# Optimization experiments

Hardware: AMD Instinct MI355X
Metric: run time of the kernel (lower is better)

## Reference

```python
import jax, jax.numpy as jnp
import numpy as np

N_STEPS = 1000
LR_INNER = 0.1
LOG_CLAMP = -100.0  # torch BCE clamps log terms at -100


def _mlp(params, x):
    h = jax.nn.sigmoid(x @ params['w1'].T + params['b1'])   # [4,16]
    return jax.nn.sigmoid(h @ params['w2'].T + params['b2'])  # [4,1]


def _bce(y_pred, y_true):
    lp = jnp.clip(jnp.log(y_pred), LOG_CLAMP)
    lq = jnp.clip(jnp.log(1.0 - y_pred), LOG_CLAMP)
    return -jnp.mean(y_true * lp + (1.0 - y_true) * lq)


def setup_inputs() -> dict:
    key = jax.random.key(0)
    k1, k2 = jax.random.split(key)
    x = jnp.array([[0.0, 0.0], [0.0, 1.0], [1.0, 0.0], [1.0, 1.0]], dtype=jnp.float32)
    y_true = jnp.array([[0.0], [1.0], [1.0], [0.0]], dtype=jnp.float32)
    return {
        'x': x,
        'y_true': y_true,
        'w1': jax.random.normal(k1, (16, 2), dtype=jnp.float32),
        'b1': jnp.zeros((16,), dtype=jnp.float32),
        'w2': jax.random.normal(k2, (1, 16), dtype=jnp.float32),
        'b2': jnp.zeros((1,), dtype=jnp.float32),
    }


def reference(x, y_true, w1, b1, w2, b2):
    params = {'w1': w1, 'b1': b1, 'w2': w2, 'b2': b2}

    def loss_fn(p):
        return _bce(_mlp(p, x), y_true)

    def step(p, _):
        loss, grads = jax.value_and_grad(loss_fn)(p)
        p_new = jax.tree_util.tree_map(lambda a, g: a - LR_INNER * g, p, grads)  # sgd
        return p_new, loss

    params, losses = jax.lax.scan(step, params, None, length=N_STEPS)
    final_output = _mlp(params, x)  # [4,1]
    return final_output, losses
```

## Files before the change

### kernel.cpp

```cpp
#include <hip/hip_runtime.h>
#include <hip/hip_bf16.h>

#define N_STEPS 1000

#define DOT_STAGE(x, N) do { float _o;                                         \
    asm("s_nop 1\n\t"                                                          \
        "v_add_f32_dpp %0, %1, %1 row_ror:" #N " row_mask:0xf bank_mask:0xf"   \
        : "=v"(_o) : "v"(x));                                                  \
    x = _o; } while (0)

#define QSUM5(q0, q1, q2, q3, q4) \
    asm("s_nop 1\n\t"                                                             \
        "v_add_f32_dpp %0, %0, %0 quad_perm:[1,0,3,2] row_mask:0xf bank_mask:0xf\n\t" \
        "v_add_f32_dpp %1, %1, %1 quad_perm:[1,0,3,2] row_mask:0xf bank_mask:0xf\n\t" \
        "v_add_f32_dpp %2, %2, %2 quad_perm:[1,0,3,2] row_mask:0xf bank_mask:0xf\n\t" \
        "v_add_f32_dpp %3, %3, %3 quad_perm:[1,0,3,2] row_mask:0xf bank_mask:0xf\n\t" \
        "v_add_f32_dpp %4, %4, %4 quad_perm:[1,0,3,2] row_mask:0xf bank_mask:0xf\n\t" \
        "v_add_f32_dpp %0, %0, %0 quad_perm:[2,3,0,1] row_mask:0xf bank_mask:0xf\n\t" \
        "v_add_f32_dpp %1, %1, %1 quad_perm:[2,3,0,1] row_mask:0xf bank_mask:0xf\n\t" \
        "v_add_f32_dpp %2, %2, %2 quad_perm:[2,3,0,1] row_mask:0xf bank_mask:0xf\n\t" \
        "v_add_f32_dpp %3, %3, %3 quad_perm:[2,3,0,1] row_mask:0xf bank_mask:0xf\n\t" \
        "v_add_f32_dpp %4, %4, %4 quad_perm:[2,3,0,1] row_mask:0xf bank_mask:0xf"     \
        : "+v"(q0), "+v"(q1), "+v"(q2), "+v"(q3), "+v"(q4))

#if defined(__has_builtin)
#  if __has_builtin(__builtin_amdgcn_permlane32_swap) && __has_builtin(__builtin_amdgcn_permlane16_swap)
#    define HAVE_PL 1
#  endif
#endif
#ifndef HAVE_PL
#  define HAVE_PL 0
#endif

template<bool PL> static __device__ __forceinline__ float redswap16(float x) {
    if (PL) {
#if HAVE_PL
        auto r = __builtin_amdgcn_permlane16_swap(__float_as_uint(x), __float_as_uint(x), false, false);
        return __uint_as_float(r[0]) + __uint_as_float(r[1]);
#endif
    }
    return x + __shfl_xor(x, 16);
}
template<bool PL> static __device__ __forceinline__ float redswap32(float x) {
    if (PL) {
#if HAVE_PL
        auto r = __builtin_amdgcn_permlane32_swap(__float_as_uint(x), __float_as_uint(x), false, false);
        return __uint_as_float(r[0]) + __uint_as_float(r[1]);
#endif
    }
    return x + __shfl_xor(x, 32);
}

#define NEG_LOG2E (-1.4426950408889634f)
#define LRS       (0.14426950408889634f)

template<bool PL>
static __device__ __forceinline__ void run_all(
    int tid, float Xr0, float Xr1, float cr,
    float Y0, float Y1, float Y2, float Y3,
    float z1s, float w2s, float B,
    float* __restrict__ p_lds, float* __restrict__ out)
{
    const float lrs_seed = (tid < 4) ? LRS : 0.0f;
    const float nC  = -0.1f;
    const float nX0 = -0.1f * Xr0;
    const float nX1 = -0.1f * Xr1;

    #pragma unroll 2
    for (int s = 0; s < N_STEPS; ++s) {
        float e1 = __builtin_amdgcn_exp2f(z1s);
        float h  = __builtin_amdgcn_rcpf(1.0f + e1);
        float vp  = (w2s * h) * (1.0f - h);
        float vX0 = vp * Xr0;
        float vX1 = vp * Xr1;

        float t = fmaf(h, w2s, B);
        DOT_STAGE(t, 4);
        DOT_STAGE(t, 8);
        t = redswap16<PL>(t);
        t = redswap32<PL>(t);
        float e2 = __builtin_amdgcn_exp2f(t);
        float p  = __builtin_amdgcn_rcpf(1.0f + e2);

        p_lds[4 * s + (tid & 3)] = p;

        float d  = fmaf(0.25f, p, cr);
        float dh = d * h;
        float u  = d * vp;
        float a0 = d * vX0;
        float a1 = d * vX1;
        QSUM5(d, dh, u, a0, a1);

        w2s = fmaf(LRS,      dh, w2s);
        B   = fmaf(lrs_seed, d,  B);
        z1s = fmaf(nC,  u,  z1s);
        z1s = fmaf(nX0, a0, z1s);
        z1s = fmaf(nX1, a1, z1s);
    }

    {
        float e1 = __builtin_amdgcn_exp2f(z1s);
        float h  = __builtin_amdgcn_rcpf(1.0f + e1);
        float t  = fmaf(h, w2s, B);
        DOT_STAGE(t, 4);
        DOT_STAGE(t, 8);
        t = redswap16<PL>(t);
        t = redswap32<PL>(t);
        float p = __builtin_amdgcn_rcpf(1.0f + __builtin_amdgcn_exp2f(t));
        if (tid < 4) out[tid] = p;
    }

    __syncthreads();

    for (int s2 = tid; s2 < N_STEPS; s2 += 64) {
        const float4 pv = *(const float4*)&p_lds[s2 * 4];
        float pp[4] = {pv.x, pv.y, pv.z, pv.w};
        float yy[4] = {Y0, Y1, Y2, Y3};
        float sum = 0.0f;
        #pragma unroll
        for (int i = 0; i < 4; ++i) {
            float pi = pp[i];
            float qi = 1.0f - pi;
            float lp = fmaxf(__logf(pi), -100.0f);
            float lq = fmaxf(__logf(qi), -100.0f);
            sum += yy[i] * lp + (1.0f - yy[i]) * lq;
        }
        out[4 + s2] = -(sum * 0.25f);
    }
}

__global__ __launch_bounds__(64, 1) void xor_train_v8(
    const void* __restrict__ x_p,
    const void* __restrict__ y_p,
    const void* __restrict__ w1_p,
    const void* __restrict__ s16a_p,
    const void* __restrict__ s16b_p,
    const void* __restrict__ b2_p,
    float* __restrict__ out)
{
    __shared__ float p_lds[N_STEPS * 4];

    const int tid = threadIdx.x;
    const int r   = tid & 3;
    const int j   = tid >> 2;

    const bool in_bf16 = (((const float*)y_p)[1] != 1.0f);
    const bool a_is_b1 = (((const unsigned*)s16a_p)[0] == 0u);
    const void* b1_p = a_is_b1 ? s16a_p : s16b_p;
    const void* w2_p = a_is_b1 ? s16b_p : s16a_p;

    float X[4][2], Y[4];
    float w10, w11, b1v, w2v, b2v;
    if (in_bf16) {
        const __hip_bfloat16* xb = (const __hip_bfloat16*)x_p;
        const __hip_bfloat16* yb = (const __hip_bfloat16*)y_p;
        #pragma unroll
        for (int i = 0; i < 4; ++i) {
            X[i][0] = __bfloat162float(xb[2 * i + 0]);
            X[i][1] = __bfloat162float(xb[2 * i + 1]);
            Y[i]    = __bfloat162float(yb[i]);
        }
        const __hip_bfloat16* w1b = (const __hip_bfloat16*)w1_p;
        w10 = __bfloat162float(w1b[2 * j + 0]);
        w11 = __bfloat162float(w1b[2 * j + 1]);
        b1v = __bfloat162float(((const __hip_bfloat16*)b1_p)[j]);
        w2v = __bfloat162float(((const __hip_bfloat16*)w2_p)[j]);
        b2v = __bfloat162float(((const __hip_bfloat16*)b2_p)[0]);
    } else {
        const float* xf = (const float*)x_p;
        const float* yf = (const float*)y_p;
        #pragma unroll
        for (int i = 0; i < 4; ++i) {
            X[i][0] = xf[2 * i + 0];
            X[i][1] = xf[2 * i + 1];
            Y[i]    = yf[i];
        }
        w10 = ((const float*)w1_p)[2 * j + 0];
        w11 = ((const float*)w1_p)[2 * j + 1];
        b1v = ((const float*)b1_p)[j];
        w2v = ((const float*)w2_p)[j];
        b2v = ((const float*)b2_p)[0];
    }

    const float Xr0 = X[r][0], Xr1 = X[r][1];
    const float cr  = -0.25f * Y[r];

    const float z1u = fmaf(Xr1, w11, fmaf(Xr0, w10, b1v));
    const float z1s = NEG_LOG2E * z1u;
    const float w2s = NEG_LOG2E * w2v;
    const float B   = (tid < 4) ? (NEG_LOG2E * b2v) : 0.0f;

    bool pl_ok = false;
#if HAVE_PL
    {
        float tv = (float)(1 << (tid >> 4));
        float fs = redswap32<true>(redswap16<true>(tv));
        pl_ok = (bool)__all(fs == 15.0f);
    }
#endif

    if (pl_ok)
        run_all<true>(tid, Xr0, Xr1, cr, Y[0], Y[1], Y[2], Y[3],
                      z1s, w2s, B, p_lds, out);
    else
        run_all<false>(tid, Xr0, Xr1, cr, Y[0], Y[1], Y[2], Y[3],
                       z1s, w2s, B, p_lds, out);
}

extern "C" void kernel_launch(void* const* d_in, const int* in_sizes, int n_in,
                              void* d_out, int out_size, void* d_ws, size_t ws_size,
                              hipStream_t stream) {
    const void* xv = nullptr; const void* yv = nullptr; const void* w1 = nullptr;
    const void* b2 = nullptr;
    const void* s16[2] = {nullptr, nullptr}; int n16 = 0;
    for (int i = 0; i < n_in; ++i) {
        switch (in_sizes[i]) {
            case 8:  xv = d_in[i]; break;
            case 4:  yv = d_in[i]; break;
            case 32: w1 = d_in[i]; break;
            case 1:  b2 = d_in[i]; break;
            case 16: if (n16 < 2) s16[n16++] = d_in[i]; break;
            default: break;
        }
    }
    if (!xv || !yv || !w1 || !b2 || n16 != 2) {
        xv = d_in[0]; yv = d_in[1]; w1 = d_in[2];
        s16[0] = d_in[3]; s16[1] = d_in[4]; b2 = d_in[5];
    }
    float* out = (float*)d_out;

    hipLaunchKernelGGL(xor_train_v8, dim3(1), dim3(64), 0, stream,
                       xv, yv, w1, s16[0], s16[1], b2, out);
}
```

Before: 118.0 us.

## Update hidden pre-activations via input Gram matrix instead of reducing gradients

Replaces the quad-wide reductions of the w1/b1 gradient terms with rotated copies of the per-row backprop term, combined through precomputed coefficients 1+x_r·x_i. This tracks the pre-activation z1 directly in input space, cutting the number of cross-lane DPP adds per step from ten to four plus three movs. It trades cross-lane reductions for an extra FMA and extra registers, and may change the rounding order slightly.

```diff
diff --git a/kernel.cpp b/kernel.cpp
--- a/kernel.cpp
+++ b/kernel.cpp
@@ -9,19 +9,18 @@
         : "=v"(_o) : "v"(x));                                                  \
     x = _o; } while (0)
 
-#define QSUM5(q0, q1, q2, q3, q4) \
-    asm("s_nop 1\n\t"                                                             \
-        "v_add_f32_dpp %0, %0, %0 quad_perm:[1,0,3,2] row_mask:0xf bank_mask:0xf\n\t" \
-        "v_add_f32_dpp %1, %1, %1 quad_perm:[1,0,3,2] row_mask:0xf bank_mask:0xf\n\t" \
-        "v_add_f32_dpp %2, %2, %2 quad_perm:[1,0,3,2] row_mask:0xf bank_mask:0xf\n\t" \
-        "v_add_f32_dpp %3, %3, %3 quad_perm:[1,0,3,2] row_mask:0xf bank_mask:0xf\n\t" \
-        "v_add_f32_dpp %4, %4, %4 quad_perm:[1,0,3,2] row_mask:0xf bank_mask:0xf\n\t" \
-        "v_add_f32_dpp %0, %0, %0 quad_perm:[2,3,0,1] row_mask:0xf bank_mask:0xf\n\t" \
-        "v_add_f32_dpp %1, %1, %1 quad_perm:[2,3,0,1] row_mask:0xf bank_mask:0xf\n\t" \
-        "v_add_f32_dpp %2, %2, %2 quad_perm:[2,3,0,1] row_mask:0xf bank_mask:0xf\n\t" \
-        "v_add_f32_dpp %3, %3, %3 quad_perm:[2,3,0,1] row_mask:0xf bank_mask:0xf\n\t" \
-        "v_add_f32_dpp %4, %4, %4 quad_perm:[2,3,0,1] row_mask:0xf bank_mask:0xf"     \
-        : "+v"(q0), "+v"(q1), "+v"(q2), "+v"(q3), "+v"(q4))
+#define BWD_XLANE(d, dh, u, u1, u2, u3) \
+    asm("s_nop 1\n\t"                                                                  \
+        "v_add_f32_dpp %[d_], %[d_], %[d_] quad_perm:[1,0,3,2] row_mask:0xf bank_mask:0xf\n\t" \
+        "v_mov_b32_dpp %[u1_], %[u_] quad_perm:[1,2,3,0] row_mask:0xf bank_mask:0xf\n\t"       \
+        "v_add_f32_dpp %[h_], %[h_], %[h_] quad_perm:[1,0,3,2] row_mask:0xf bank_mask:0xf\n\t" \
+        "v_mov_b32_dpp %[u2_], %[u_] quad_perm:[2,3,0,1] row_mask:0xf bank_mask:0xf\n\t"       \
+        "v_mov_b32_dpp %[u3_], %[u_] quad_perm:[3,0,1,2] row_mask:0xf bank_mask:0xf\n\t"       \
+        "v_add_f32_dpp %[d_], %[d_], %[d_] quad_perm:[2,3,0,1] row_mask:0xf bank_mask:0xf\n\t" \
+        "v_add_f32_dpp %[h_], %[h_], %[h_] quad_perm:[2,3,0,1] row_mask:0xf bank_mask:0xf"     \
+        : [d_] "+v"(d), [h_] "+v"(dh),                                                 \
+          [u1_] "=&v"(u1), [u2_] "=&v"(u2), [u3_] "=&v"(u3)                            \
+        : [u_] "v"(u))
 
 #if defined(__has_builtin)
 #  if __has_builtin(__builtin_amdgcn_permlane32_swap) && __has_builtin(__builtin_amdgcn_permlane16_swap)
@@ -57,22 +56,18 @@
 template<bool PL>
 static __device__ __forceinline__ void run_all(
     int tid, float Xr0, float Xr1, float cr,
+    float M0, float M1, float M2, float M3,
     float Y0, float Y1, float Y2, float Y3,
     float z1s, float w2s, float B,
     float* __restrict__ p_lds, float* __restrict__ out)
 {
     const float lrs_seed = (tid < 4) ? LRS : 0.0f;
-    const float nC  = -0.1f;
-    const float nX0 = -0.1f * Xr0;
-    const float nX1 = -0.1f * Xr1;
 
     #pragma unroll 2
     for (int s = 0; s < N_STEPS; ++s) {
         float e1 = __builtin_amdgcn_exp2f(z1s);
         float h  = __builtin_amdgcn_rcpf(1.0f + e1);
-        float vp  = (w2s * h) * (1.0f - h);
-        float vX0 = vp * Xr0;
-        float vX1 = vp * Xr1;
+        float vp = (w2s * h) * (1.0f - h);
 
         float t = fmaf(h, w2s, B);
         DOT_STAGE(t, 4);
@@ -85,17 +80,17 @@
         p_lds[4 * s + (tid & 3)] = p;
 
         float d  = fmaf(0.25f, p, cr);
+        float u  = d * vp;
         float dh = d * h;
-        float u  = d * vp;
-        float a0 = d * vX0;
-        float a1 = d * vX1;
-        QSUM5(d, dh, u, a0, a1);
-
+        float u1, u2, u3;
+        BWD_XLANE(d, dh, u, u1, u2, u3);
+
+        z1s = fmaf(M0, u,  z1s);
+        z1s = fmaf(M1, u1, z1s);
+        z1s = fmaf(M2, u2, z1s);
+        z1s = fmaf(M3, u3, z1s);
         w2s = fmaf(LRS,      dh, w2s);
         B   = fmaf(lrs_seed, d,  B);
-        z1s = fmaf(nC,  u,  z1s);
-        z1s = fmaf(nX0, a0, z1s);
-        z1s = fmaf(nX1, a1, z1s);
     }
 
     {
@@ -129,7 +124,7 @@
     }
 }
 
-__global__ __launch_bounds__(64, 1) void xor_train_v8(
+__global__ __launch_bounds__(64, 1) void xor_train_v9(
     const void* __restrict__ x_p,
     const void* __restrict__ y_p,
     const void* __restrict__ w1_p,
@@ -185,6 +180,14 @@
     const float Xr0 = X[r][0], Xr1 = X[r][1];
     const float cr  = -0.25f * Y[r];
 
+    const int r1 = (r + 1) & 3, r2 = (r + 2) & 3, r3 = (r + 3) & 3;
+    #define SELX(idx, c) ((idx) == 0 ? X[0][c] : (idx) == 1 ? X[1][c] : (idx) == 2 ? X[2][c] : X[3][c])
+    const float M0 = -0.1f * (1.0f + Xr0 * Xr0 + Xr1 * Xr1);
+    const float M1 = -0.1f * (1.0f + Xr0 * SELX(r1, 0) + Xr1 * SELX(r1, 1));
+    const float M2 = -0.1f * (1.0f + Xr0 * SELX(r2, 0) + Xr1 * SELX(r2, 1));
+    const float M3 = -0.1f * (1.0f + Xr0 * SELX(r3, 0) + Xr1 * SELX(r3, 1));
+    #undef SELX
+
     const float z1u = fmaf(Xr1, w11, fmaf(Xr0, w10, b1v));
     const float z1s = NEG_LOG2E * z1u;
     const float w2s = NEG_LOG2E * w2v;
@@ -200,11 +203,11 @@
 #endif
 
     if (pl_ok)
-        run_all<true>(tid, Xr0, Xr1, cr, Y[0], Y[1], Y[2], Y[3],
-                      z1s, w2s, B, p_lds, out);
+        run_all<true>(tid, Xr0, Xr1, cr, M0, M1, M2, M3,
+                      Y[0], Y[1], Y[2], Y[3], z1s, w2s, B, p_lds, out);
     else
-        run_all<false>(tid, Xr0, Xr1, cr, Y[0], Y[1], Y[2], Y[3],
-                       z1s, w2s, B, p_lds, out);
+        run_all<false>(tid, Xr0, Xr1, cr, M0, M1, M2, M3,
+                       Y[0], Y[1], Y[2], Y[3], z1s, w2s, B, p_lds, out);
 }
 
 extern "C" void kernel_launch(void* const* d_in, const int* in_sizes, int n_in,
@@ -229,6 +232,6 @@
     }
     float* out = (float*)d_out;
 
-    hipLaunchKernelGGL(xor_train_v8, dim3(1), dim3(64), 0, stream,
+    hipLaunchKernelGGL(xor_train_v9, dim3(1), dim3(64), 0, stream,
                        xv, yv, w1, s16[0], s16[1], b2, out);
 }
```

Result: faster. 111.6 us (-5.4%).
